# Optimization experiments

Measured on AMD Instinct MI355X. Metric: run time of the kernel, lower is better.

Reference implementation:

```python
import jax, jax.numpy as jnp
import numpy as np

N_NODES = 100000
N_EDGES = 1200000
D = 64
H = D * D  # GRUCell hidden size = 4096


def gru_cell(x, h, w_ih, w_hh, b_ih, b_hh):
    # torch.nn.GRUCell, unbatched vectors x,h of shape (H,)
    gx = w_ih @ x + b_ih            # (3H,)
    gh = w_hh @ h + b_hh
    xr, xz, xn = jnp.split(gx, 3)
    hr, hz, hn = jnp.split(gh, 3)
    r = jax.nn.sigmoid(xr + hr)
    z = jax.nn.sigmoid(xz + hz)
    n = jnp.tanh(xn + r * hn)
    return (1.0 - z) * n + z * h


def graph_conv(x, src, dst, w, b):
    # DGL GraphConv norm='both': D_out^{-1/2} on src, aggregate, D_in^{-1/2} on dst
    ones = jnp.ones((src.shape[0],), dtype=x.dtype)
    deg_out = jnp.clip(jax.ops.segment_sum(ones, src, num_segments=N_NODES), 1.0)
    deg_in = jnp.clip(jax.ops.segment_sum(ones, dst, num_segments=N_NODES), 1.0)
    h = (x * jax.lax.rsqrt(deg_out)[:, None]) @ w          # [N, D]
    agg = jax.ops.segment_sum(h[src], dst, num_segments=N_NODES)  # SpMM gather/scatter
    return agg * jax.lax.rsqrt(deg_in)[:, None] + b


def setup_inputs() -> dict:
    key = jax.random.key(0)
    ks = jax.random.split(key, 10)
    scale = 1.0 / np.sqrt(H)
    return {
        "node_embeddings": jax.random.normal(ks[0], (N_NODES, D), jnp.float32),
        "src": jax.random.randint(ks[1], (N_EDGES,), 0, N_NODES, jnp.int32),
        "dst": jax.random.randint(ks[2], (N_EDGES,), 0, N_NODES, jnp.int32),
        "gc1_weight": jax.random.normal(ks[3], (D, D), jnp.float32) * (1.0 / np.sqrt(D)),
        "gc1_bias": jnp.zeros((D,), jnp.float32),
        "gc2_weight": jax.random.normal(ks[4], (D, D), jnp.float32) * (1.0 / np.sqrt(D)),
        "gc2_bias": jnp.zeros((D,), jnp.float32),
        "gc1_hist": jax.random.normal(ks[5], (D, D), jnp.float32) * (1.0 / np.sqrt(D)),
        "gc2_hist": jax.random.normal(ks[6], (D, D), jnp.float32) * (1.0 / np.sqrt(D)),
        "gru_w_ih": jax.random.normal(ks[7], (3 * H, H), jnp.float32) * scale,
        "gru_w_hh": jax.random.normal(ks[8], (3 * H, H), jnp.float32) * scale,
        "gru_b_ih": jnp.zeros((3 * H,), jnp.float32),
        "gru_b_hh": jnp.zeros((3 * H,), jnp.float32),
    }


def reference(node_embeddings, src, dst, gc1_weight, gc1_bias, gc2_weight, gc2_bias,
              gc1_hist, gc2_hist, gru_w_ih, gru_w_hh, gru_b_ih, gru_b_hh):
    # weight evolution: GRU(input=history, hidden=current weight)
    w1 = gru_cell(gc1_hist.reshape(-1), gc1_weight.reshape(-1),
                  gru_w_ih, gru_w_hh, gru_b_ih, gru_b_hh).reshape(D, D)
    w2 = gru_cell(gc2_hist.reshape(-1), gc2_weight.reshape(-1),
                  gru_w_ih, gru_w_hh, gru_b_ih, gru_b_hh).reshape(D, D)
    x = jax.nn.relu(graph_conv(node_embeddings, src, dst, w1, gc1_bias))
    x = graph_conv(x, src, dst, w2, gc2_bias)
    return x
```

## Files before the change

kernel.cpp:

```cpp
#include <hip/hip_runtime.h>
#include <math.h>

#define N_NODES 100000
#define N_EDGES 1200000
#define DD 64
#define HH 4096
#define H3 12288
#define NB_SCAN 98

__global__ void zero_i4(int4* __restrict__ p, int n4) {
    int i = blockIdx.x * blockDim.x + threadIdx.x;
    if (i < n4) p[i] = make_int4(0, 0, 0, 0);
}

__global__ void hist_kernel(const int* __restrict__ src, const int* __restrict__ dst,
                            int* __restrict__ hs, int* __restrict__ hd) {
    int i = blockIdx.x * blockDim.x + threadIdx.x;
    int stride = gridDim.x * blockDim.x;
    for (int e = i; e < N_EDGES; e += stride) {
        atomicAdd(&hs[src[e]], 1);
        atomicAdd(&hd[dst[e]], 1);
    }
}

__global__ void rsqrt_from_hist(const int* __restrict__ hs, const int* __restrict__ hd,
                                float* __restrict__ rs_out, float* __restrict__ rs_in) {
    int i = blockIdx.x * blockDim.x + threadIdx.x;
    if (i < N_NODES) {
        rs_out[i] = rsqrtf(fmaxf((float)hs[i], 1.0f));
        rs_in[i]  = rsqrtf(fmaxf((float)hd[i], 1.0f));
    }
}

__global__ __launch_bounds__(256) void scan1(const int* __restrict__ hist, int* __restrict__ offs,
                                             int* __restrict__ bsum) {
    __shared__ int wsum[4];
    int b = blockIdx.x;
    int base = b * 1024;
    int t = threadIdx.x;
    int idx = base + t * 4;
    int v0 = 0, v1 = 0, v2 = 0, v3 = 0;
    if (idx + 0 < N_NODES) v0 = hist[idx + 0];
    if (idx + 1 < N_NODES) v1 = hist[idx + 1];
    if (idx + 2 < N_NODES) v2 = hist[idx + 2];
    if (idx + 3 < N_NODES) v3 = hist[idx + 3];
    int s = v0 + v1 + v2 + v3;
    int lane = t & 63, wv = t >> 6;
    int sc = s;
#pragma unroll
    for (int off = 1; off < 64; off <<= 1) {
        int n = __shfl_up(sc, off);
        if (lane >= off) sc += n;
    }
    if (lane == 63) wsum[wv] = sc;
    __syncthreads();
    int wadd = 0;
    for (int i = 0; i < wv; ++i) wadd += wsum[i];
    int excl = wadd + sc - s;
    if (idx + 0 < N_NODES) offs[idx + 0] = excl;
    if (idx + 1 < N_NODES) offs[idx + 1] = excl + v0;
    if (idx + 2 < N_NODES) offs[idx + 2] = excl + v0 + v1;
    if (idx + 3 < N_NODES) offs[idx + 3] = excl + v0 + v1 + v2;
    if (t == 255) bsum[b] = wadd + sc;
}

__global__ void scan2(int* __restrict__ bsum) {
    if (threadIdx.x == 0 && blockIdx.x == 0) {
        int acc = 0;
        for (int i = 0; i < NB_SCAN; ++i) { int v = bsum[i]; bsum[i] = acc; acc += v; }
    }
}

__global__ void scan3(int* __restrict__ offs, const int* __restrict__ bsum,
                      int* __restrict__ cursor) {
    int i = blockIdx.x * blockDim.x + threadIdx.x;
    if (i < N_NODES) {
        int o = offs[i] + bsum[i >> 10];
        offs[i] = o;
        cursor[i] = o;
    } else if (i == N_NODES) {
        offs[N_NODES] = N_EDGES;
    }
}

__global__ void reorder_kernel(const int* __restrict__ src, const int* __restrict__ dst,
                               int* __restrict__ cursor, int* __restrict__ ssort) {
    int e = blockIdx.x * blockDim.x + threadIdx.x;
    if (e < N_EDGES) {
        int d = dst[e];
        int p = atomicAdd(&cursor[d], 1);
        ssort[p] = src[e];
    }
}

__global__ __launch_bounds__(256) void gru_matvec(
        const float* __restrict__ w_ih, const float* __restrict__ w_hh,
        const float* __restrict__ x1, const float* __restrict__ x2,
        const float* __restrict__ h1, const float* __restrict__ h2,
        float* __restrict__ gbuf) {
    int wave = (blockIdx.x * blockDim.x + threadIdx.x) >> 6;
    int lane = threadIdx.x & 63;
    int mat  = wave / H3;
    int row  = wave - mat * H3;
    const float4* M  = (const float4*)((mat ? w_hh : w_ih) + (size_t)row * HH);
    const float4* va = (const float4*)(mat ? h1 : x1);
    const float4* vb = (const float4*)(mat ? h2 : x2);
    float acc_a = 0.f, acc_b = 0.f;
#pragma unroll
    for (int i = 0; i < 16; ++i) {
        float4 m = M[lane + i * 64];
        float4 a = va[lane + i * 64];
        float4 b = vb[lane + i * 64];
        acc_a += m.x * a.x + m.y * a.y + m.z * a.z + m.w * a.w;
        acc_b += m.x * b.x + m.y * b.y + m.z * b.z + m.w * b.w;
    }
#pragma unroll
    for (int off = 32; off > 0; off >>= 1) {
        acc_a += __shfl_xor(acc_a, off);
        acc_b += __shfl_xor(acc_b, off);
    }
    if (lane == 0) {
        gbuf[(mat * 2 + 0) * H3 + row] = acc_a;
        gbuf[(mat * 2 + 1) * H3 + row] = acc_b;
    }
}

__global__ void gru_combine(const float* __restrict__ gbuf,
                            const float* __restrict__ b_ih, const float* __restrict__ b_hh,
                            const float* __restrict__ w1_cur, const float* __restrict__ w2_cur,
                            float* __restrict__ wevo) {
    int j = blockIdx.x * blockDim.x + threadIdx.x;
    if (j >= 2 * HH) return;
    int layer = j >> 12;
    int jj = j & (HH - 1);
    const float* gx = gbuf + layer * H3;
    const float* gh = gbuf + (2 + layer) * H3;
    float xr = gx[jj] + b_ih[jj];
    float xz = gx[HH + jj] + b_ih[HH + jj];
    float xn = gx[2 * HH + jj] + b_ih[2 * HH + jj];
    float hr = gh[jj] + b_hh[jj];
    float hz = gh[HH + jj] + b_hh[HH + jj];
    float hn = gh[2 * HH + jj] + b_hh[2 * HH + jj];
    float h = (layer ? w2_cur : w1_cur)[jj];
    float r = 1.0f / (1.0f + expf(-(xr + hr)));
    float z = 1.0f / (1.0f + expf(-(xz + hz)));
    float n = tanhf(xn + r * hn);
    wevo[layer * HH + jj] = (1.0f - z) * n + z * h;
}

__global__ __launch_bounds__(256) void gemm64(
        const float* __restrict__ in, const float* __restrict__ w,
        float* __restrict__ out, const float* __restrict__ rs_out,
        const float* __restrict__ rs_in, const float* __restrict__ bias, int mode) {
    __shared__ float wl[HH];
    __shared__ float xs[4][DD];
    for (int i = threadIdx.x; i < HH; i += 256) wl[i] = w[i];
    int wv = threadIdx.x >> 6, lane = threadIdx.x & 63;
    int r = blockIdx.x * 4 + wv;
    float v = in[(size_t)r * DD + lane];
    if (mode) v = fmaxf(fmaf(v, rs_in[r], bias[lane]), 0.0f);
    v *= rs_out[r];
    xs[wv][lane] = v;
    __syncthreads();
    float acc = 0.f;
#pragma unroll
    for (int k = 0; k < DD; ++k) acc = fmaf(xs[wv][k], wl[k * DD + lane], acc);
    out[(size_t)r * DD + lane] = acc;
}

__global__ __launch_bounds__(256) void agg_kernel(
        const float* __restrict__ h, const int* __restrict__ ssort,
        const int* __restrict__ offs, const float* __restrict__ rs_in,
        const float* __restrict__ bias, float* __restrict__ outp, int mode) {
    int wv = threadIdx.x >> 6, lane = threadIdx.x & 63;
    int r = blockIdx.x * 4 + wv;
    int start = offs[r], end = offs[r + 1];
    float acc = 0.f;
    int e = start;
    while (e < end) {
        int cnt = min(end - e, 64);
        int s = (lane < cnt) ? ssort[e + lane] : 0;
        for (int i = 0; i < cnt; ++i) {
            int si = __shfl(s, i);
            acc += h[(size_t)si * DD + lane];
        }
        e += cnt;
    }
    if (mode) acc = fmaf(acc, rs_in[r], bias[lane]);
    outp[(size_t)r * DD + lane] = acc;
}

extern "C" void kernel_launch(void* const* d_in, const int* in_sizes, int n_in,
                              void* d_out, int out_size, void* d_ws, size_t ws_size,
                              hipStream_t stream) {
    const float* node_emb   = (const float*)d_in[0];
    const int*   src        = (const int*)d_in[1];
    const int*   dst        = (const int*)d_in[2];
    const float* gc1_weight = (const float*)d_in[3];
    const float* gc1_bias   = (const float*)d_in[4];
    const float* gc2_weight = (const float*)d_in[5];
    const float* gc2_bias   = (const float*)d_in[6];
    const float* gc1_hist   = (const float*)d_in[7];
    const float* gc2_hist   = (const float*)d_in[8];
    const float* w_ih       = (const float*)d_in[9];
    const float* w_hh       = (const float*)d_in[10];
    const float* b_ih       = (const float*)d_in[11];
    const float* b_hh       = (const float*)d_in[12];
    float* out = (float*)d_out;

    float* ws     = (float*)d_ws;
    float* rs_out = ws;
    float* rs_in  = ws + N_NODES;
    float* gbuf   = ws + 2 * N_NODES;
    float* wevo   = gbuf + 4 * H3;
    float* agg    = wevo + 2 * HH;
    int*   hs     = (int*)(agg + (size_t)N_NODES * DD);
    int*   hd     = hs + N_NODES;
    int*   offs   = hd + N_NODES;
    int*   cursor = offs + N_NODES + 1;
    int*   bsum   = cursor + N_NODES;
    int*   ssort  = bsum + 128;

    zero_i4<<<(2 * N_NODES / 4 + 255) / 256, 256, 0, stream>>>((int4*)hs, 2 * N_NODES / 4);
    hist_kernel<<<2048, 256, 0, stream>>>(src, dst, hs, hd);
    rsqrt_from_hist<<<(N_NODES + 255) / 256, 256, 0, stream>>>(hs, hd, rs_out, rs_in);
    scan1<<<NB_SCAN, 256, 0, stream>>>(hd, offs, bsum);
    scan2<<<1, 64, 0, stream>>>(bsum);
    scan3<<<(N_NODES + 256) / 256, 256, 0, stream>>>(offs, bsum, cursor);
    reorder_kernel<<<(N_EDGES + 255) / 256, 256, 0, stream>>>(src, dst, cursor, ssort);

    gru_matvec<<<6144, 256, 0, stream>>>(w_ih, w_hh, gc1_hist, gc2_hist,
                                         gc1_weight, gc2_weight, gbuf);
    gru_combine<<<32, 256, 0, stream>>>(gbuf, b_ih, b_hh, gc1_weight, gc2_weight, wevo);

    gemm64<<<25000, 256, 0, stream>>>(node_emb, wevo, out, rs_out, rs_in, gc1_bias, 0);
    agg_kernel<<<25000, 256, 0, stream>>>(out, ssort, offs, rs_in, gc1_bias, agg, 0);

    gemm64<<<25000, 256, 0, stream>>>(agg, wevo + HH, agg, rs_out, rs_in, gc1_bias, 1);
    agg_kernel<<<25000, 256, 0, stream>>>(agg, ssort, offs, rs_in, gc2_bias, out, 1);
}
```

Measured before the change: 886.9 us.

## Fuse layer-1 aggregation with layer-2 GEMM and vectorize edge gathers

Merges the first aggregation with the second layer's normalize/ReLU/matmul into one kernel, which removes a kernel launch and a full N×64 round trip through memory. Both aggregation kernels now use float4 gathers, with four sub-groups of 16 lanes each walking a different edge and combining through shuffles, in place of the per-edge broadcast loop. The GRU matvec stages its input vectors in shared memory and software-pipelines the weight loads. The weight copies into shared memory use float4. In exchange, sub-group lanes sit idle when a node has few edges, and the staging adds per-block overhead.

```diff
diff --git a/kernel.cpp b/kernel.cpp
--- a/kernel.cpp
+++ b/kernel.cpp
@@ -98,21 +98,36 @@
         const float* __restrict__ x1, const float* __restrict__ x2,
         const float* __restrict__ h1, const float* __restrict__ h2,
         float* __restrict__ gbuf) {
-    int wave = (blockIdx.x * blockDim.x + threadIdx.x) >> 6;
-    int lane = threadIdx.x & 63;
-    int mat  = wave / H3;
-    int row  = wave - mat * H3;
-    const float4* M  = (const float4*)((mat ? w_hh : w_ih) + (size_t)row * HH);
-    const float4* va = (const float4*)(mat ? h1 : x1);
-    const float4* vb = (const float4*)(mat ? h2 : x2);
+    __shared__ float4 va_s[1024];
+    __shared__ float4 vb_s[1024];
+    int mat = blockIdx.x >= 3072;
+    const float4* vaG = (const float4*)(mat ? h1 : x1);
+    const float4* vbG = (const float4*)(mat ? h2 : x2);
+    for (int i = threadIdx.x; i < 1024; i += 256) {
+        va_s[i] = vaG[i];
+        vb_s[i] = vbG[i];
+    }
+    __syncthreads();
+    int wv = threadIdx.x >> 6, lane = threadIdx.x & 63;
+    int row = (mat ? blockIdx.x - 3072 : blockIdx.x) * 4 + wv;
+    const float4* M = (const float4*)((mat ? w_hh : w_ih) + (size_t)row * HH);
     float acc_a = 0.f, acc_b = 0.f;
-#pragma unroll
-    for (int i = 0; i < 16; ++i) {
-        float4 m = M[lane + i * 64];
-        float4 a = va[lane + i * 64];
-        float4 b = vb[lane + i * 64];
-        acc_a += m.x * a.x + m.y * a.y + m.z * a.z + m.w * a.w;
-        acc_b += m.x * b.x + m.y * b.y + m.z * b.z + m.w * b.w;
+    float4 m0 = M[lane];
+    float4 m1 = M[lane + 64];
+#pragma unroll
+    for (int i = 0; i < 8; ++i) {
+        float4 n0, n1;
+        if (i < 7) {
+            n0 = M[lane + (i + 1) * 128];
+            n1 = M[lane + (i + 1) * 128 + 64];
+        }
+        float4 a0 = va_s[lane + i * 128], a1 = va_s[lane + i * 128 + 64];
+        float4 b0 = vb_s[lane + i * 128], b1 = vb_s[lane + i * 128 + 64];
+        acc_a += m0.x * a0.x + m0.y * a0.y + m0.z * a0.z + m0.w * a0.w
+               + m1.x * a1.x + m1.y * a1.y + m1.z * a1.z + m1.w * a1.w;
+        acc_b += m0.x * b0.x + m0.y * b0.y + m0.z * b0.z + m0.w * b0.w
+               + m1.x * b1.x + m1.y * b1.y + m1.z * b1.z + m1.w * b1.w;
+        if (i < 7) { m0 = n0; m1 = n1; }
     }
 #pragma unroll
     for (int off = 32; off > 0; off >>= 1) {
@@ -150,16 +165,13 @@
 
 __global__ __launch_bounds__(256) void gemm64(
         const float* __restrict__ in, const float* __restrict__ w,
-        float* __restrict__ out, const float* __restrict__ rs_out,
-        const float* __restrict__ rs_in, const float* __restrict__ bias, int mode) {
+        float* __restrict__ out, const float* __restrict__ rs_out) {
     __shared__ float wl[HH];
     __shared__ float xs[4][DD];
-    for (int i = threadIdx.x; i < HH; i += 256) wl[i] = w[i];
+    for (int i = threadIdx.x; i < 1024; i += 256) ((float4*)wl)[i] = ((const float4*)w)[i];
     int wv = threadIdx.x >> 6, lane = threadIdx.x & 63;
     int r = blockIdx.x * 4 + wv;
-    float v = in[(size_t)r * DD + lane];
-    if (mode) v = fmaxf(fmaf(v, rs_in[r], bias[lane]), 0.0f);
-    v *= rs_out[r];
+    float v = in[(size_t)r * DD + lane] * rs_out[r];
     xs[wv][lane] = v;
     __syncthreads();
     float acc = 0.f;
@@ -168,26 +180,79 @@
     out[(size_t)r * DD + lane] = acc;
 }
 
-__global__ __launch_bounds__(256) void agg_kernel(
+__global__ __launch_bounds__(256) void agg_gemm(
+        const float* __restrict__ h, const int* __restrict__ ssort,
+        const int* __restrict__ offs, const float* __restrict__ rs_out,
+        const float* __restrict__ rs_in, const float* __restrict__ bias,
+        const float* __restrict__ w, float* __restrict__ outp) {
+    __shared__ float wl[HH];
+    __shared__ float xs[4][DD];
+    for (int i = threadIdx.x; i < 1024; i += 256) ((float4*)wl)[i] = ((const float4*)w)[i];
+    int wv = threadIdx.x >> 6, lane = threadIdx.x & 63;
+    int sub = lane >> 4, c4 = lane & 15;
+    int r = blockIdx.x * 4 + wv;
+    int start = offs[r], end = offs[r + 1];
+    float4 acc = make_float4(0.f, 0.f, 0.f, 0.f);
+    for (int e = start + sub; e < end; e += 4) {
+        int s = ssort[e];
+        float4 v = *(const float4*)(h + (size_t)s * DD + c4 * 4);
+        acc.x += v.x; acc.y += v.y; acc.z += v.z; acc.w += v.w;
+    }
+#pragma unroll
+    for (int off = 16; off <= 32; off <<= 1) {
+        acc.x += __shfl_xor(acc.x, off);
+        acc.y += __shfl_xor(acc.y, off);
+        acc.z += __shfl_xor(acc.z, off);
+        acc.w += __shfl_xor(acc.w, off);
+    }
+    float ri = rs_in[r], ro = rs_out[r];
+    float4 bb = *(const float4*)(bias + c4 * 4);
+    if (sub == 0) {
+        float4 v;
+        v.x = fmaxf(fmaf(acc.x, ri, bb.x), 0.f) * ro;
+        v.y = fmaxf(fmaf(acc.y, ri, bb.y), 0.f) * ro;
+        v.z = fmaxf(fmaf(acc.z, ri, bb.z), 0.f) * ro;
+        v.w = fmaxf(fmaf(acc.w, ri, bb.w), 0.f) * ro;
+        *(float4*)(&xs[wv][c4 * 4]) = v;
+    }
+    __syncthreads();
+    float o = 0.f;
+#pragma unroll
+    for (int k = 0; k < DD; ++k) o = fmaf(xs[wv][k], wl[k * DD + lane], o);
+    outp[(size_t)r * DD + lane] = o;
+}
+
+__global__ __launch_bounds__(256) void agg_final(
         const float* __restrict__ h, const int* __restrict__ ssort,
         const int* __restrict__ offs, const float* __restrict__ rs_in,
-        const float* __restrict__ bias, float* __restrict__ outp, int mode) {
+        const float* __restrict__ bias, float* __restrict__ outp) {
     int wv = threadIdx.x >> 6, lane = threadIdx.x & 63;
+    int sub = lane >> 4, c4 = lane & 15;
     int r = blockIdx.x * 4 + wv;
     int start = offs[r], end = offs[r + 1];
-    float acc = 0.f;
-    int e = start;
-    while (e < end) {
-        int cnt = min(end - e, 64);
-        int s = (lane < cnt) ? ssort[e + lane] : 0;
-        for (int i = 0; i < cnt; ++i) {
-            int si = __shfl(s, i);
-            acc += h[(size_t)si * DD + lane];
-        }
-        e += cnt;
-    }
-    if (mode) acc = fmaf(acc, rs_in[r], bias[lane]);
-    outp[(size_t)r * DD + lane] = acc;
+    float4 acc = make_float4(0.f, 0.f, 0.f, 0.f);
+    for (int e = start + sub; e < end; e += 4) {
+        int s = ssort[e];
+        float4 v = *(const float4*)(h + (size_t)s * DD + c4 * 4);
+        acc.x += v.x; acc.y += v.y; acc.z += v.z; acc.w += v.w;
+    }
+#pragma unroll
+    for (int off = 16; off <= 32; off <<= 1) {
+        acc.x += __shfl_xor(acc.x, off);
+        acc.y += __shfl_xor(acc.y, off);
+        acc.z += __shfl_xor(acc.z, off);
+        acc.w += __shfl_xor(acc.w, off);
+    }
+    if (sub == 0) {
+        float ri = rs_in[r];
+        float4 bb = *(const float4*)(bias + c4 * 4);
+        float4 v;
+        v.x = fmaf(acc.x, ri, bb.x);
+        v.y = fmaf(acc.y, ri, bb.y);
+        v.z = fmaf(acc.z, ri, bb.z);
+        v.w = fmaf(acc.w, ri, bb.w);
+        *(float4*)(outp + (size_t)r * DD + c4 * 4) = v;
+    }
 }
 
 extern "C" void kernel_launch(void* const* d_in, const int* in_sizes, int n_in,
@@ -233,9 +298,8 @@
                                          gc1_weight, gc2_weight, gbuf);
     gru_combine<<<32, 256, 0, stream>>>(gbuf, b_ih, b_hh, gc1_weight, gc2_weight, wevo);
 
-    gemm64<<<25000, 256, 0, stream>>>(node_emb, wevo, out, rs_out, rs_in, gc1_bias, 0);
-    agg_kernel<<<25000, 256, 0, stream>>>(out, ssort, offs, rs_in, gc1_bias, agg, 0);
-
-    gemm64<<<25000, 256, 0, stream>>>(agg, wevo + HH, agg, rs_out, rs_in, gc1_bias, 1);
-    agg_kernel<<<25000, 256, 0, stream>>>(agg, ssort, offs, rs_in, gc2_bias, out, 1);
-}
+    gemm64<<<25000, 256, 0, stream>>>(node_emb, wevo, out, rs_out);
+    agg_gemm<<<25000, 256, 0, stream>>>(out, ssort, offs, rs_out, rs_in, gc1_bias,
+                                        wevo + HH, agg);
+    agg_final<<<25000, 256, 0, stream>>>(agg, ssort, offs, rs_in, gc2_bias, out);
+}
```

Measured after the change: 795.6 us. 10.3% less time.
